# Performance work log

Hardware: AMD Instinct MI355X
Metric: run time of the kernel (lower is better)

The kernel has to match this reference:

```python
import jax, jax.numpy as jnp
import numpy as np

HEADS = 8
CH = 64  # channel_head
SCALE = CH ** -0.5


def rmsnorm2d(x, g):
    # F.normalize(x, dim=1) * g * sqrt(C)  (lucidrains conv RMSNorm)
    c = x.shape[1]
    n = jnp.sqrt(jnp.sum(x * x, axis=1, keepdims=True))
    return x / jnp.maximum(n, 1e-12) * g[None, :, None, None] * (c ** 0.5)


def setup_inputs() -> dict:
    key = jax.random.key(0)
    ks = jax.random.split(key, 3)
    B, C, H, W = 8, 512, 64, 64
    hidden = HEADS * CH  # 512
    x = jax.random.normal(ks[0], (B, C, H, W), dtype=jnp.float32)
    norm_g = jnp.ones((C,), dtype=jnp.float32)
    qkv_w = jax.random.normal(ks[1], (3 * hidden, C), dtype=jnp.float32) * 0.02
    ffn_w = jax.random.normal(ks[2], (C, hidden), dtype=jnp.float32) * 0.02
    ffn_b = jnp.zeros((C,), dtype=jnp.float32)
    ffn_norm_g = jnp.ones((C,), dtype=jnp.float32)
    return {"x": x, "norm_g": norm_g, "qkv_w": qkv_w, "ffn_w": ffn_w,
            "ffn_b": ffn_b, "ffn_norm_g": ffn_norm_g}


def reference(x, norm_g, qkv_w, ffn_w, ffn_b, ffn_norm_g):
    b, c, h, w = x.shape
    n = h * w
    residual = x
    xn = rmsnorm2d(x, norm_g)
    # 1x1 conv == channel matmul: [b, 3*hidden, h, w]
    qkv = jnp.einsum('bchw,oc->bohw', xn, qkv_w)
    q, k, v = jnp.split(qkv, 3, axis=1)

    def to_heads(t):
        # b (h c) x y -> b h (x y) c
        t = t.reshape(b, HEADS, CH, n)
        return jnp.transpose(t, (0, 1, 3, 2))  # [b, heads, n, ch]

    q, k, v = to_heads(q), to_heads(k), to_heads(v)
    q = jax.nn.softmax(q, axis=-1) * SCALE   # softmax over channel dim
    k = jax.nn.softmax(k, axis=-2)           # softmax over sequence dim
    attn = jnp.einsum('bhnc,bhnd->bhcd', k, v)    # [b, heads, ch, ch]
    out = jnp.einsum('bhnc,bhcd->bhnd', q, attn)  # [b, heads, n, ch]
    # b h (x y) c -> b (h c) x y
    out = jnp.transpose(out, (0, 1, 3, 2)).reshape(b, HEADS * CH, h, w)
    # ffn: 1x1 conv (with bias) + RMSNorm
    out = jnp.einsum('bchw,oc->bohw', out, ffn_w) + ffn_b[None, :, None, None]
    out = rmsnorm2d(out, ffn_norm_g)
    return out + residual
```

## Files before the change

kernel.cpp:

```cpp
#include <hip/hip_runtime.h>


typedef __bf16 bf16_t;
typedef __bf16 bf8 __attribute__((ext_vector_type(8)));
typedef float f32x4 __attribute__((ext_vector_type(4)));

#define NC 512
#define NP 4096
#define SQRTC 22.62741699796952f
#define QSCALE 0.125f
#define QSTRIDE  ((size_t)NC * NP)
#define KVSTRIDE ((size_t)1024 * NP)
#define LDC 136

__device__ inline unsigned short bfbits(__bf16 h) {
    return __builtin_bit_cast(unsigned short, h);
}

__device__ __forceinline__ void gload_lds16(const bf16_t* g, __bf16* l) {
    __builtin_amdgcn_global_load_lds(
        (const __attribute__((address_space(1))) void*)g,
        (__attribute__((address_space(3))) void*)l, 16, 0, 0);
}

__global__ __launch_bounds__(256) void
wconv_kernel(const float* __restrict__ qkv_w, const float* __restrict__ g,
             const float* __restrict__ ffn_w, bf16_t* __restrict__ Wg,
             bf16_t* __restrict__ Wf) {
    const int bx = blockIdx.x;
    if (bx < 768) {
        int i0 = (bx * 256 + threadIdx.x) * 4;
        float4 wv = *(const float4*)&qkv_w[i0];
        const float4 gv = *(const float4*)&g[i0 & 511];
        ushort4 o;
        o.x = bfbits((__bf16)(wv.x * gv.x));
        o.y = bfbits((__bf16)(wv.y * gv.y));
        o.z = bfbits((__bf16)(wv.z * gv.z));
        o.w = bfbits((__bf16)(wv.w * gv.w));
        *(ushort4*)&Wg[i0] = o;
    } else {
        int i0 = ((bx - 768) * 256 + threadIdx.x) * 4;
        float4 wv = *(const float4*)&ffn_w[i0];
        ushort4 o;
        o.x = bfbits((__bf16)wv.x);
        o.y = bfbits((__bf16)wv.y);
        o.z = bfbits((__bf16)wv.z);
        o.w = bfbits((__bf16)wv.w);
        *(ushort4*)&Wf[i0] = o;
    }
}

__global__ __launch_bounds__(512) void
norm_transpose_kernel(const float* __restrict__ x, bf16_t* __restrict__ xnT,
                      const float* __restrict__ qkv_w, const float* __restrict__ g,
                      const float* __restrict__ ffn_w, bf16_t* __restrict__ Wg,
                      bf16_t* __restrict__ Wf, int doW) {
    const int bl = blockIdx.y;
    const int p0 = blockIdx.x * 32;
    const int t = threadIdx.x;

    if (doW) {
        const int bid = blockIdx.y * 128 + blockIdx.x;
        if (bid < 512) {
            int i0 = bid * 2048 + t * 4;
            if (i0 < 786432) {
                float4 wv = *(const float4*)&qkv_w[i0];
                const float4 gv = *(const float4*)&g[i0 & 511];
                ushort4 o;
                o.x = bfbits((__bf16)(wv.x * gv.x));
                o.y = bfbits((__bf16)(wv.y * gv.y));
                o.z = bfbits((__bf16)(wv.z * gv.z));
                o.w = bfbits((__bf16)(wv.w * gv.w));
                *(ushort4*)&Wg[i0] = o;
            } else {
                int j0 = i0 - 786432;
                float4 wv = *(const float4*)&ffn_w[j0];
                ushort4 o;
                o.x = bfbits((__bf16)wv.x);
                o.y = bfbits((__bf16)wv.y);
                o.z = bfbits((__bf16)wv.z);
                o.w = bfbits((__bf16)wv.w);
                *(ushort4*)&Wf[j0] = o;
            }
        }
    }

    const float* xb = x + (size_t)bl * QSTRIDE;
    bf16_t* ob = xnT + (size_t)bl * QSTRIDE;

    const int cg = t & 7, r0 = t >> 3;
    f32x4 ss = {0.f, 0.f, 0.f, 0.f};
    #pragma unroll
    for (int k = 0; k < 8; ++k) {
        const int c = r0 + k * 64;
        float4 v = *(const float4*)&xb[(size_t)c * NP + p0 + cg * 4];
        ss.x += v.x * v.x; ss.y += v.y * v.y;
        ss.z += v.z * v.z; ss.w += v.w * v.w;
    }
    #pragma unroll
    for (int m = 8; m <= 32; m <<= 1) {
        ss.x += __shfl_xor(ss.x, m); ss.y += __shfl_xor(ss.y, m);
        ss.z += __shfl_xor(ss.z, m); ss.w += __shfl_xor(ss.w, m);
    }
    __shared__ float sP[8][34];
    __shared__ float sInv[32];
    const int w = t >> 6;
    if ((t & 63) < 8) {
        const int p = (t & 7) * 4;
        sP[w][p] = ss.x; sP[w][p + 1] = ss.y;
        sP[w][p + 2] = ss.z; sP[w][p + 3] = ss.w;
    }
    __syncthreads();
    if (t < 32) {
        float tot = 0.f;
        #pragma unroll
        for (int j = 0; j < 8; ++j) tot += sP[j][t];
        sInv[t] = SQRTC / fmaxf(sqrtf(tot), 1e-12f);
    }
    __syncthreads();

    __shared__ __bf16 sT[128][41];
    for (int cc = 0; cc < 512; cc += 128) {
        #pragma unroll
        for (int j = 0; j < 2; ++j) {
            int idx = t + j * 512;
            int cr = idx >> 3, pg = idx & 7;
            float4 v = *(const float4*)&xb[(size_t)(cc + cr) * NP + p0 + pg * 4];
            sT[cr][pg * 4 + 0] = (__bf16)(v.x * sInv[pg * 4 + 0]);
            sT[cr][pg * 4 + 1] = (__bf16)(v.y * sInv[pg * 4 + 1]);
            sT[cr][pg * 4 + 2] = (__bf16)(v.z * sInv[pg * 4 + 2]);
            sT[cr][pg * 4 + 3] = (__bf16)(v.w * sInv[pg * 4 + 3]);
        }
        __syncthreads();
        {
            int p = t >> 4, c8 = (t & 15) * 8;
            bf8 v;
            #pragma unroll
            for (int q = 0; q < 8; ++q) v[q] = sT[c8 + q][p];
            *(bf8*)&ob[(size_t)(p0 + p) * NC + cc + c8] = v;
        }
        __syncthreads();
    }
}

__global__ __launch_bounds__(256) void
gemm_qkv_kernel(const bf16_t* __restrict__ Wg, const bf16_t* __restrict__ xnT,
                bf16_t* __restrict__ qout, bf16_t* __restrict__ kvout) {
    const int bn = blockIdx.x, bm = blockIdx.y, b = blockIdx.z;
    const int t = threadIdx.x;
    const int w = t >> 6, ln = t & 63, quad = ln >> 4, l16 = ln & 15;
    const int wm = w >> 1, wn = w & 1;

    __shared__ __align__(16) __bf16 sAB[128 * LDC];
    __bf16* const sA = sAB;
    __bf16* const sB = sAB + 8192;

    f32x4 acc[4][4] = {};
    const bf16_t* Abase = Wg + (size_t)(bm * 128) * NC;
    const bf16_t* Bbase = xnT + (size_t)b * QSTRIDE + (size_t)(bn * 128) * NC;

    const int lrow = ln >> 3;
    const int lkc = ((ln & 7) ^ lrow) * 8;
    const int xr = l16 & 7;

    for (int kt = 0; kt < 8; ++kt) {
        const int k0 = kt * 64;
        #pragma unroll
        for (int i = 0; i < 4; ++i) {
            const int chunk = w * 4 + i;
            const int row = chunk * 8 + lrow;
            gload_lds16(Abase + (size_t)row * NC + k0 + lkc, &sA[chunk * 512]);
            gload_lds16(Bbase + (size_t)row * NC + k0 + lkc, &sB[chunk * 512]);
        }
        __syncthreads();
        #pragma unroll
        for (int ks = 0; ks < 2; ++ks) {
            bf8 af[4], bfr[4];
            const int kx = ((ks * 4 + quad) ^ xr) << 3;
            #pragma unroll
            for (int mi = 0; mi < 4; ++mi)
                af[mi] = *(const bf8*)&sA[(wm * 64 + mi * 16 + l16) * 64 + kx];
            #pragma unroll
            for (int ni = 0; ni < 4; ++ni)
                bfr[ni] = *(const bf8*)&sB[(wn * 64 + ni * 16 + l16) * 64 + kx];
            #pragma unroll
            for (int mi = 0; mi < 4; ++mi)
                #pragma unroll
                for (int ni = 0; ni < 4; ++ni)
                    acc[mi][ni] = __builtin_amdgcn_mfma_f32_16x16x32_bf16(
                        af[mi], bfr[ni], acc[mi][ni], 0, 0, 0);
        }
        __syncthreads();
    }

    const int p0 = bn * 128;
    if (bm < 4) {
        #pragma unroll
        for (int mi = 0; mi < 4; ++mi)
            #pragma unroll
            for (int ni = 0; ni < 4; ++ni)
                #pragma unroll
                for (int r = 0; r < 4; ++r)
                    sAB[(wn * 64 + ni * 16 + l16) * LDC +
                        wm * 64 + mi * 16 + quad * 4 + r] = (__bf16)acc[mi][ni][r];
        __syncthreads();
        {
            __bf16* rp = &sAB[(t & 127) * LDC + (t >> 7) * 64];
            float m = -1e30f;
            #pragma unroll
            for (int gg = 0; gg < 8; ++gg) {
                bf8 v = *(const bf8*)&rp[gg * 8];
                #pragma unroll
                for (int j = 0; j < 8; ++j) m = fmaxf(m, (float)v[j]);
            }
            float s = 0.f;
            #pragma unroll
            for (int gg = 0; gg < 8; ++gg) {
                bf8 v = *(const bf8*)&rp[gg * 8];
                #pragma unroll
                for (int j = 0; j < 8; ++j) s += __expf((float)v[j] - m);
            }
            const float inv = QSCALE / s;
            #pragma unroll
            for (int gg = 0; gg < 8; ++gg) {
                bf8 v = *(const bf8*)&rp[gg * 8];
                #pragma unroll
                for (int j = 0; j < 8; ++j)
                    v[j] = (__bf16)(__expf((float)v[j] - m) * inv);
                *(bf8*)&rp[gg * 8] = v;
            }
        }
        __syncthreads();
        bf16_t* qb = qout + (size_t)b * QSTRIDE;
        #pragma unroll
        for (int i = 0; i < 8; ++i) {
            int e = t + i * 256;
            int p = e >> 4, c8 = (e & 15) * 8;
            bf8 v = *(const bf8*)&sAB[p * LDC + c8];
            *(bf8*)&qb[(size_t)(p0 + p) * NC + bm * 128 + c8] = v;
        }
    } else {
        {
            const int rbase = wm * 64 + quad * 4;
            const int cbase = wn * 64 + l16;
            #pragma unroll
            for (int mi = 0; mi < 4; ++mi)
                #pragma unroll
                for (int ni = 0; ni < 4; ++ni)
                    #pragma unroll
                    for (int r = 0; r < 4; ++r)
                        sAB[(rbase + mi * 16 + r) * LDC + cbase + ni * 16] =
                            (__bf16)acc[mi][ni][r];
        }
        __syncthreads();
        bf16_t* kvb = kvout + (size_t)b * KVSTRIDE;
        #pragma unroll
        for (int i = 0; i < 8; ++i) {
            int e = t + i * 256;
            int rr = e >> 4, seg = (e & 15) * 8;
            bf8 v = *(const bf8*)&sAB[rr * LDC + seg];
            *(bf8*)&kvb[(size_t)(bm * 128 + rr - 512) * NP + p0 + seg] = v;
        }
    }
}

__global__ __launch_bounds__(256) void
kstats_kernel(const bf16_t* __restrict__ kv, float* __restrict__ kmax,
              float* __restrict__ kinv) {
    const int oc = blockIdx.x, b = blockIdx.y;
    const int t = threadIdx.x, w = t >> 6, ln = t & 63;

    const bf16_t* row = kv + (size_t)b * KVSTRIDE + (size_t)oc * NP;
    float v[16];
    bf8 x0 = *(const bf8*)&row[t * 8];
    bf8 x1 = *(const bf8*)&row[2048 + t * 8];
    #pragma unroll
    for (int j = 0; j < 8; ++j) { v[j] = (float)x0[j]; v[8 + j] = (float)x1[j]; }

    float m = v[0];
    #pragma unroll
    for (int j = 1; j < 16; ++j) m = fmaxf(m, v[j]);
    #pragma unroll
    for (int off = 32; off > 0; off >>= 1) m = fmaxf(m, __shfl_down(m, off));
    __shared__ float sR[4];
    __shared__ float sS[4];
    if (ln == 0) sR[w] = m;
    __syncthreads();
    m = fmaxf(fmaxf(sR[0], sR[1]), fmaxf(sR[2], sR[3]));

    float s = 0.f;
    #pragma unroll
    for (int j = 0; j < 16; ++j) s += __expf(v[j] - m);
    #pragma unroll
    for (int off = 32; off > 0; off >>= 1) s += __shfl_down(s, off);
    if (ln == 0) sS[w] = s;
    __syncthreads();
    if (t == 0) {
        kmax[b * 512 + oc] = m;
        kinv[b * 512 + oc] = 1.0f / (sS[0] + sS[1] + sS[2] + sS[3]);
    }
}

__global__ __launch_bounds__(256) void
attn_kernel(const bf16_t* __restrict__ kv, const float* __restrict__ kmax,
            float* __restrict__ attnP) {
    const int h = blockIdx.x, ks = blockIdx.y, b = blockIdx.z;
    const int t = threadIdx.x, w = t >> 6, ln = t & 63, quad = ln >> 4, l16 = ln & 15;

    const bf16_t* Kb = kv + (size_t)b * KVSTRIDE + (size_t)(h * 64) * NP;
    const bf16_t* Vb = kv + (size_t)b * KVSTRIDE + (size_t)(512 + h * 64 + w * 16) * NP;

    float km[4];
    #pragma unroll
    for (int mi = 0; mi < 4; ++mi) km[mi] = kmax[b * 512 + h * 64 + mi * 16 + l16];

    f32x4 acc[4] = {};
    const int pbase = ks * 512 + quad * 8;
    #pragma unroll 4
    for (int it = 0; it < 16; ++it) {
        const int p0 = pbase + it * 32;
        bf8 bfr = *(const bf8*)&Vb[(size_t)l16 * NP + p0];
        #pragma unroll
        for (int mi = 0; mi < 4; ++mi) {
            bf8 kr = *(const bf8*)&Kb[(size_t)(mi * 16 + l16) * NP + p0];
            bf8 af;
            #pragma unroll
            for (int j = 0; j < 8; ++j)
                af[j] = (__bf16)__expf((float)kr[j] - km[mi]);
            acc[mi] = __builtin_amdgcn_mfma_f32_16x16x32_bf16(af, bfr, acc[mi], 0, 0, 0);
        }
    }

    float* outp = attnP + (((size_t)(b * 8 + h) * 8 + ks) << 12);
    #pragma unroll
    for (int mi = 0; mi < 4; ++mi) {
        float4 v;
        v.x = acc[mi][0]; v.y = acc[mi][1]; v.z = acc[mi][2]; v.w = acc[mi][3];
        *(float4*)&outp[(w * 16 + l16) * 64 + mi * 16 + quad * 4] = v;
    }
}

__global__ __launch_bounds__(256) void
attnsum_kernel(const float* __restrict__ attnP, const float* __restrict__ kinv,
               bf16_t* __restrict__ attnF, float* __restrict__ ysq) {
    const int gtid = (blockIdx.x * 4 + blockIdx.y) * 256 + threadIdx.x;
    if (gtid < 8 * NP) ysq[gtid] = 0.f;

    const int bh = blockIdx.x;
    const int e0 = blockIdx.y * 1024 + threadIdx.x * 4;
    const float* ap = attnP + ((size_t)bh << 15);
    float4 s = {0.f, 0.f, 0.f, 0.f};
    #pragma unroll
    for (int ks = 0; ks < 8; ++ks) {
        float4 v = *(const float4*)&ap[(ks << 12) + e0];
        s.x += v.x; s.y += v.y; s.z += v.z; s.w += v.w;
    }
    const float* kvp = kinv + (bh >> 3) * 512 + (bh & 7) * 64;
    const int c = e0 & 63;
    ushort4 o;
    o.x = bfbits((__bf16)(s.x * kvp[c]));
    o.y = bfbits((__bf16)(s.y * kvp[c + 1]));
    o.z = bfbits((__bf16)(s.z * kvp[c + 2]));
    o.w = bfbits((__bf16)(s.w * kvp[c + 3]));
    *(ushort4*)&attnF[((size_t)bh << 12) + e0] = o;
}

__global__ __launch_bounds__(256) void
wmix_kernel(const bf16_t* __restrict__ Wf, const bf16_t* __restrict__ attnF,
            bf16_t* __restrict__ Wff) {
    const int om = blockIdx.x, h = blockIdx.y, b = blockIdx.z;
    const int t = threadIdx.x, w = t >> 6, ln = t & 63, quad = ln >> 4, l16 = ln & 15;

    __shared__ __bf16 sT[64][72];
    const bf16_t* aF = attnF + ((size_t)(b * 8 + h) << 12);
    #pragma unroll
    for (int i = 0; i < 2; ++i) {
        int e = t + i * 256;
        int d = e >> 3, c8 = (e & 7) * 8;
        bf8 v = *(const bf8*)&aF[d * 64 + c8];
        #pragma unroll
        for (int j = 0; j < 8; ++j) sT[c8 + j][d] = v[j];
    }
    __syncthreads();

    const int obase = om * 128 + w * 32;
    f32x4 acc[2][4] = {};
    #pragma unroll
    for (int kk = 0; kk < 2; ++kk) {
        bf8 af[2], bfr[4];
        #pragma unroll
        for (int mi = 0; mi < 2; ++mi)
            af[mi] = *(const bf8*)&Wf[(size_t)(obase + mi * 16 + l16) * NC +
                                      h * 64 + kk * 32 + quad * 8];
        #pragma unroll
        for (int ni = 0; ni < 4; ++ni)
            bfr[ni] = *(const bf8*)&sT[ni * 16 + l16][kk * 32 + quad * 8];
        #pragma unroll
        for (int mi = 0; mi < 2; ++mi)
            #pragma unroll
            for (int ni = 0; ni < 4; ++ni)
                acc[mi][ni] = __builtin_amdgcn_mfma_f32_16x16x32_bf16(
                    af[mi], bfr[ni], acc[mi][ni], 0, 0, 0);
    }
    bf16_t* outp = Wff + ((size_t)b << 18);
    #pragma unroll
    for (int mi = 0; mi < 2; ++mi)
        #pragma unroll
        for (int ni = 0; ni < 4; ++ni)
            #pragma unroll
            for (int r = 0; r < 4; ++r) {
                int o = obase + mi * 16 + quad * 4 + r;
                int c = ni * 16 + l16;
                outp[(size_t)o * NC + h * 64 + c] = (__bf16)acc[mi][ni][r];
            }
}

__global__ __launch_bounds__(256) void
gemm_ffn_kernel(const bf16_t* __restrict__ Wff, const bf16_t* __restrict__ qsm,
                const float* __restrict__ bias, float* __restrict__ out,
                float* __restrict__ ysq) {
    const int bn = blockIdx.x, bm = blockIdx.y, b = blockIdx.z;
    const int t = threadIdx.x;
    const int w = t >> 6, ln = t & 63, quad = ln >> 4, l16 = ln & 15;
    const int wm = w >> 1, wn = w & 1;

    __shared__ __align__(16) __bf16 sAB[128 * LDC];
    __bf16* const sA = sAB;
    __bf16* const sB = sAB + 8192;

    f32x4 acc[4][4] = {};
    const bf16_t* Abase = Wff + ((size_t)b << 18) + (size_t)(bm * 128) * NC;
    const bf16_t* Bbase = qsm + (size_t)b * QSTRIDE + (size_t)(bn * 128) * NC;

    const int lrow = ln >> 3;
    const int lkc = ((ln & 7) ^ lrow) * 8;
    const int xr = l16 & 7;

    for (int kt = 0; kt < 8; ++kt) {
        const int k0 = kt * 64;
        #pragma unroll
        for (int i = 0; i < 4; ++i) {
            const int chunk = w * 4 + i;
            const int row = chunk * 8 + lrow;
            gload_lds16(Abase + (size_t)row * NC + k0 + lkc, &sA[chunk * 512]);
            gload_lds16(Bbase + (size_t)row * NC + k0 + lkc, &sB[chunk * 512]);
        }
        __syncthreads();
        #pragma unroll
        for (int ks = 0; ks < 2; ++ks) {
            bf8 af[4], bfr[4];
            const int kx = ((ks * 4 + quad) ^ xr) << 3;
            #pragma unroll
            for (int mi = 0; mi < 4; ++mi)
                af[mi] = *(const bf8*)&sA[(wm * 64 + mi * 16 + l16) * 64 + kx];
            #pragma unroll
            for (int ni = 0; ni < 4; ++ni)
                bfr[ni] = *(const bf8*)&sB[(wn * 64 + ni * 16 + l16) * 64 + kx];
            #pragma unroll
            for (int mi = 0; mi < 4; ++mi)
                #pragma unroll
                for (int ni = 0; ni < 4; ++ni)
                    acc[mi][ni] = __builtin_amdgcn_mfma_f32_16x16x32_bf16(
                        af[mi], bfr[ni], acc[mi][ni], 0, 0, 0);
        }
        __syncthreads();
    }

    float* sq = ysq + (size_t)b * NP;
    const int p0 = bn * 128;
    const int rbase = wm * 64 + quad * 4;
    #pragma unroll
    for (int ni = 0; ni < 4; ++ni) {
        const int col = p0 + wn * 64 + ni * 16 + l16;
        float colsq = 0.f;
        #pragma unroll
        for (int mi = 0; mi < 4; ++mi)
            #pragma unroll
            for (int r = 0; r < 4; ++r) {
                float vf = acc[mi][ni][r] + bias[bm * 128 + rbase + mi * 16 + r];
                colsq += vf * vf;
            }
        colsq += __shfl_xor(colsq, 16);
        colsq += __shfl_xor(colsq, 32);
        if (quad == 0) atomicAdd(&sq[col], colsq);
    }

    float* sF = (float*)sAB;
    float* ob = out + (size_t)b * QSTRIDE;
    #pragma unroll
    for (int half = 0; half < 2; ++half) {
        __syncthreads();
        if (wm == half) {
            #pragma unroll
            for (int mi = 0; mi < 4; ++mi)
                #pragma unroll
                for (int ni = 0; ni < 4; ++ni)
                    #pragma unroll
                    for (int r = 0; r < 4; ++r)
                        sF[(quad * 4 + mi * 16 + r) * 136 + wn * 64 + ni * 16 + l16] =
                            acc[mi][ni][r] +
                            bias[bm * 128 + half * 64 + quad * 4 + mi * 16 + r];
        }
        __syncthreads();
        #pragma unroll
        for (int i = 0; i < 8; ++i) {
            int e = t + i * 256;
            int rr = e >> 5, c4 = (e & 31) * 4;
            float4 v = *(const float4*)&sF[rr * 136 + c4];
            *(float4*)&ob[(size_t)(bm * 128 + half * 64 + rr) * NP + p0 + c4] = v;
        }
    }
}

__global__ __launch_bounds__(256) void
final_kernel(float* __restrict__ out, const float* __restrict__ ysq,
             const float* __restrict__ g2, const float* __restrict__ x) {
    const int b = blockIdx.y;
    int idx = blockIdx.x * 256 + threadIdx.x;
    int o = idx >> 9;
    int p8 = (idx & 511) * 8;
    float* ob = out + (size_t)b * QSTRIDE;
    const float* xb = x + (size_t)b * QSTRIDE;
    const float* sq = ysq + (size_t)b * NP;

    float4 y0 = *(const float4*)&ob[(size_t)o * NP + p8];
    float4 y1 = *(const float4*)&ob[(size_t)o * NP + p8 + 4];
    float gv = g2[o] * SQRTC;
    float4 a = *(const float4*)&xb[(size_t)o * NP + p8];
    float4 b2 = *(const float4*)&xb[(size_t)o * NP + p8 + 4];
    float inb[8];
    #pragma unroll
    for (int j = 0; j < 8; ++j)
        inb[j] = 1.0f / fmaxf(sqrtf(sq[p8 + j]), 1e-12f);

    float4 r0, r1;
    r0.x = y0.x * inb[0] * gv + a.x;
    r0.y = y0.y * inb[1] * gv + a.y;
    r0.z = y0.z * inb[2] * gv + a.z;
    r0.w = y0.w * inb[3] * gv + a.w;
    r1.x = y1.x * inb[4] * gv + b2.x;
    r1.y = y1.y * inb[5] * gv + b2.y;
    r1.z = y1.z * inb[6] * gv + b2.z;
    r1.w = y1.w * inb[7] * gv + b2.w;
    *(float4*)&ob[(size_t)o * NP + p8] = r0;
    *(float4*)&ob[(size_t)o * NP + p8 + 4] = r1;
}

extern "C" void kernel_launch(void* const* d_in, const int* in_sizes, int n_in,
                              void* d_out, int out_size, void* d_ws, size_t ws_size,
                              hipStream_t stream) {
    const float* x     = (const float*)d_in[0];
    const float* g     = (const float*)d_in[1];
    const float* qkv_w = (const float*)d_in[2];
    const float* ffn_w = (const float*)d_in[3];
    const float* ffn_b = (const float*)d_in[4];
    const float* ffn_g = (const float*)d_in[5];
    float* out = (float*)d_out;
    bf16_t* kv = (bf16_t*)d_out;

    const size_t FULL_BYTES =
        (8 * QSTRIDE + 8 * QSTRIDE + 786432 + 262144) * sizeof(bf16_t) +
        (8 * 512 + 8 * 512 + 8 * (size_t)NP) * sizeof(float);
    const bool full = ws_size >= FULL_BYTES;

    bf16_t* q    = (bf16_t*)d_ws;
    bf16_t* xnT  = q + 8 * QSTRIDE;
    bf16_t* Wg   = xnT + (full ? 8 : 2) * QSTRIDE;
    float*  attnP = (float*)xnT;
    bf16_t* attnF = Wg;
    bf16_t* Wff  = xnT;
    bf16_t* Wf   = Wg + 786432;
    float*  kmax = (float*)(Wf + 262144);
    float*  kinv = kmax + 8 * 512;
    float*  ysq  = kinv + 8 * 512;

    if (full) {
        norm_transpose_kernel<<<dim3(128, 8), 512, 0, stream>>>(
            x, xnT, qkv_w, g, ffn_w, Wg, Wf, 1);
        gemm_qkv_kernel<<<dim3(32, 12, 8), 256, 0, stream>>>(Wg, xnT, q, kv);
    } else {
        wconv_kernel<<<dim3(1024), 256, 0, stream>>>(qkv_w, g, ffn_w, Wg, Wf);
        for (int c = 0; c < 4; ++c) {
            norm_transpose_kernel<<<dim3(128, 2), 512, 0, stream>>>(
                x + (size_t)(2 * c) * QSTRIDE, xnT,
                qkv_w, g, ffn_w, Wg, Wf, 0);
            gemm_qkv_kernel<<<dim3(32, 12, 2), 256, 0, stream>>>(
                Wg, xnT, q + (size_t)(2 * c) * QSTRIDE,
                kv + (size_t)(2 * c) * KVSTRIDE);
        }
    }

    kstats_kernel<<<dim3(512, 8), 256, 0, stream>>>(kv, kmax, kinv);
    attn_kernel<<<dim3(8, 8, 8), 256, 0, stream>>>(kv, kmax, attnP);
    attnsum_kernel<<<dim3(64, 4), 256, 0, stream>>>(attnP, kinv, attnF, ysq);
    wmix_kernel<<<dim3(4, 8, 8), 256, 0, stream>>>(Wf, attnF, Wff);
    gemm_ffn_kernel<<<dim3(32, 4, 8), 256, 0, stream>>>(Wff, q, ffn_b, out, ysq);
    final_kernel<<<dim3(1024, 8), 256, 0, stream>>>(out, ysq, ffn_g, x);
}
```

Measured before the change: 304.3 us.

## Fold attnsum into wmix, zero ysq in attn, store FFN output as bf16

On the full-workspace path, the separate attnsum launch is removed. The partial-attention reduction and kinv scaling move into wmix_kernel, and attn_kernel now zeroes ysq. The FFN GEMM writes its pre-norm output as bf16 to workspace instead of fp32 to the output buffer, and the column sum-of-squares is computed from the rounded values. This halves the intermediate write and read in final_kernel at the cost of bf16 rounding of the pre-norm activations, and it places Wff in the kv region.

```diff
diff --git a/kernel.cpp b/kernel.cpp
--- a/kernel.cpp
+++ b/kernel.cpp
@@ -303,9 +303,12 @@
 
 __global__ __launch_bounds__(256) void
 attn_kernel(const bf16_t* __restrict__ kv, const float* __restrict__ kmax,
-            float* __restrict__ attnP) {
+            float* __restrict__ attnP, float* __restrict__ ysq) {
     const int h = blockIdx.x, ks = blockIdx.y, b = blockIdx.z;
     const int t = threadIdx.x, w = t >> 6, ln = t & 63, quad = ln >> 4, l16 = ln & 15;
+
+    const int zid = ((b * 8 + ks) * 8 + h) * 256 + t;
+    if (zid < 8 * NP) ysq[zid] = 0.f;
 
     const bf16_t* Kb = kv + (size_t)b * KVSTRIDE + (size_t)(h * 64) * NP;
     const bf16_t* Vb = kv + (size_t)b * KVSTRIDE + (size_t)(512 + h * 64 + w * 16) * NP;
@@ -366,20 +369,43 @@
 }
 
 __global__ __launch_bounds__(256) void
-wmix_kernel(const bf16_t* __restrict__ Wf, const bf16_t* __restrict__ attnF,
-            bf16_t* __restrict__ Wff) {
+wmix_kernel(const bf16_t* __restrict__ Wf, const float* __restrict__ attnP,
+            const float* __restrict__ kinv, const bf16_t* __restrict__ attnF,
+            bf16_t* __restrict__ Wff, int selfsum) {
     const int om = blockIdx.x, h = blockIdx.y, b = blockIdx.z;
     const int t = threadIdx.x, w = t >> 6, ln = t & 63, quad = ln >> 4, l16 = ln & 15;
 
     __shared__ __bf16 sT[64][72];
-    const bf16_t* aF = attnF + ((size_t)(b * 8 + h) << 12);
-    #pragma unroll
-    for (int i = 0; i < 2; ++i) {
-        int e = t + i * 256;
-        int d = e >> 3, c8 = (e & 7) * 8;
-        bf8 v = *(const bf8*)&aF[d * 64 + c8];
-        #pragma unroll
-        for (int j = 0; j < 8; ++j) sT[c8 + j][d] = v[j];
+    if (selfsum) {
+        const float* ap = attnP + ((size_t)(b * 8 + h) << 15);
+        const float* kvp = kinv + b * 512 + h * 64;
+        #pragma unroll
+        for (int i = 0; i < 2; ++i) {
+            int e = t + i * 256;
+            int d = e >> 3, c8 = (e & 7) * 8;
+            float s[8] = {};
+            #pragma unroll
+            for (int ks = 0; ks < 8; ++ks) {
+                const float* pp = &ap[(ks << 12) + d * 64 + c8];
+                float4 v0 = *(const float4*)pp;
+                float4 v1 = *(const float4*)(pp + 4);
+                s[0] += v0.x; s[1] += v0.y; s[2] += v0.z; s[3] += v0.w;
+                s[4] += v1.x; s[5] += v1.y; s[6] += v1.z; s[7] += v1.w;
+            }
+            #pragma unroll
+            for (int j = 0; j < 8; ++j)
+                sT[c8 + j][d] = (__bf16)(s[j] * kvp[c8 + j]);
+        }
+    } else {
+        const bf16_t* aF = attnF + ((size_t)(b * 8 + h) << 12);
+        #pragma unroll
+        for (int i = 0; i < 2; ++i) {
+            int e = t + i * 256;
+            int d = e >> 3, c8 = (e & 7) * 8;
+            bf8 v = *(const bf8*)&aF[d * 64 + c8];
+            #pragma unroll
+            for (int j = 0; j < 8; ++j) sT[c8 + j][d] = v[j];
+        }
     }
     __syncthreads();
 
@@ -417,8 +443,8 @@
 
 __global__ __launch_bounds__(256) void
 gemm_ffn_kernel(const bf16_t* __restrict__ Wff, const bf16_t* __restrict__ qsm,
-                const float* __restrict__ bias, float* __restrict__ out,
-                float* __restrict__ ysq) {
+                const float* __restrict__ bias, float* __restrict__ outf,
+                bf16_t* __restrict__ ybf16, float* __restrict__ ysq, int ybf) {
     const int bn = blockIdx.x, bm = blockIdx.y, b = blockIdx.z;
     const int t = threadIdx.x;
     const int w = t >> 6, ln = t & 63, quad = ln >> 4, l16 = ln & 15;
@@ -469,52 +495,84 @@
     float* sq = ysq + (size_t)b * NP;
     const int p0 = bn * 128;
     const int rbase = wm * 64 + quad * 4;
-    #pragma unroll
-    for (int ni = 0; ni < 4; ++ni) {
-        const int col = p0 + wn * 64 + ni * 16 + l16;
-        float colsq = 0.f;
-        #pragma unroll
-        for (int mi = 0; mi < 4; ++mi)
-            #pragma unroll
-            for (int r = 0; r < 4; ++r) {
-                float vf = acc[mi][ni][r] + bias[bm * 128 + rbase + mi * 16 + r];
-                colsq += vf * vf;
-            }
-        colsq += __shfl_xor(colsq, 16);
-        colsq += __shfl_xor(colsq, 32);
-        if (quad == 0) atomicAdd(&sq[col], colsq);
-    }
-
-    float* sF = (float*)sAB;
-    float* ob = out + (size_t)b * QSTRIDE;
-    #pragma unroll
-    for (int half = 0; half < 2; ++half) {
-        __syncthreads();
-        if (wm == half) {
-            #pragma unroll
-            for (int mi = 0; mi < 4; ++mi)
-                #pragma unroll
-                for (int ni = 0; ni < 4; ++ni)
-                    #pragma unroll
-                    for (int r = 0; r < 4; ++r)
-                        sF[(quad * 4 + mi * 16 + r) * 136 + wn * 64 + ni * 16 + l16] =
-                            acc[mi][ni][r] +
-                            bias[bm * 128 + half * 64 + quad * 4 + mi * 16 + r];
-        }
-        __syncthreads();
+
+    if (ybf) {
+        #pragma unroll
+        for (int ni = 0; ni < 4; ++ni) {
+            const int col = p0 + wn * 64 + ni * 16 + l16;
+            float colsq = 0.f;
+            #pragma unroll
+            for (int mi = 0; mi < 4; ++mi) {
+                #pragma unroll
+                for (int r = 0; r < 4; ++r) {
+                    const int row = bm * 128 + rbase + mi * 16 + r;
+                    __bf16 vb = (__bf16)(acc[mi][ni][r] + bias[row]);
+                    sAB[(rbase + mi * 16 + r) * LDC + wn * 64 + ni * 16 + l16] = vb;
+                    float vf = (float)vb;
+                    colsq += vf * vf;
+                }
+            }
+            colsq += __shfl_xor(colsq, 16);
+            colsq += __shfl_xor(colsq, 32);
+            if (quad == 0) atomicAdd(&sq[col], colsq);
+        }
+        __syncthreads();
+        bf16_t* yb = ybf16 + (size_t)b * QSTRIDE;
         #pragma unroll
         for (int i = 0; i < 8; ++i) {
             int e = t + i * 256;
-            int rr = e >> 5, c4 = (e & 31) * 4;
-            float4 v = *(const float4*)&sF[rr * 136 + c4];
-            *(float4*)&ob[(size_t)(bm * 128 + half * 64 + rr) * NP + p0 + c4] = v;
-        }
-    }
-}
-
-__global__ __launch_bounds__(256) void
-final_kernel(float* __restrict__ out, const float* __restrict__ ysq,
-             const float* __restrict__ g2, const float* __restrict__ x) {
+            int rr = e >> 4, seg = (e & 15) * 8;
+            bf8 v = *(const bf8*)&sAB[rr * LDC + seg];
+            *(bf8*)&yb[(size_t)(bm * 128 + rr) * NP + p0 + seg] = v;
+        }
+    } else {
+        #pragma unroll
+        for (int ni = 0; ni < 4; ++ni) {
+            const int col = p0 + wn * 64 + ni * 16 + l16;
+            float colsq = 0.f;
+            #pragma unroll
+            for (int mi = 0; mi < 4; ++mi)
+                #pragma unroll
+                for (int r = 0; r < 4; ++r) {
+                    float vf = acc[mi][ni][r] + bias[bm * 128 + rbase + mi * 16 + r];
+                    colsq += vf * vf;
+                }
+            colsq += __shfl_xor(colsq, 16);
+            colsq += __shfl_xor(colsq, 32);
+            if (quad == 0) atomicAdd(&sq[col], colsq);
+        }
+        float* sF = (float*)sAB;
+        float* ob = outf + (size_t)b * QSTRIDE;
+        #pragma unroll
+        for (int half = 0; half < 2; ++half) {
+            __syncthreads();
+            if (wm == half) {
+                #pragma unroll
+                for (int mi = 0; mi < 4; ++mi)
+                    #pragma unroll
+                    for (int ni = 0; ni < 4; ++ni)
+                        #pragma unroll
+                        for (int r = 0; r < 4; ++r)
+                            sF[(quad * 4 + mi * 16 + r) * 136 + wn * 64 + ni * 16 + l16] =
+                                acc[mi][ni][r] +
+                                bias[bm * 128 + half * 64 + quad * 4 + mi * 16 + r];
+            }
+            __syncthreads();
+            #pragma unroll
+            for (int i = 0; i < 8; ++i) {
+                int e = t + i * 256;
+                int rr = e >> 5, c4 = (e & 31) * 4;
+                float4 v = *(const float4*)&sF[rr * 136 + c4];
+                *(float4*)&ob[(size_t)(bm * 128 + half * 64 + rr) * NP + p0 + c4] = v;
+            }
+        }
+    }
+}
+
+__global__ __launch_bounds__(256) void
+final_kernel(float* __restrict__ out, const bf16_t* __restrict__ ybf16,
+             const float* __restrict__ ysq, const float* __restrict__ g2,
+             const float* __restrict__ x, int ybf) {
     const int b = blockIdx.y;
     int idx = blockIdx.x * 256 + threadIdx.x;
     int o = idx >> 9;
@@ -523,8 +581,6 @@
     const float* xb = x + (size_t)b * QSTRIDE;
     const float* sq = ysq + (size_t)b * NP;
 
-    float4 y0 = *(const float4*)&ob[(size_t)o * NP + p8];
-    float4 y1 = *(const float4*)&ob[(size_t)o * NP + p8 + 4];
     float gv = g2[o] * SQRTC;
     float4 a = *(const float4*)&xb[(size_t)o * NP + p8];
     float4 b2 = *(const float4*)&xb[(size_t)o * NP + p8 + 4];
@@ -533,15 +589,28 @@
     for (int j = 0; j < 8; ++j)
         inb[j] = 1.0f / fmaxf(sqrtf(sq[p8 + j]), 1e-12f);
 
+    float y[8];
+    if (ybf) {
+        const bf16_t* yb = ybf16 + (size_t)b * QSTRIDE;
+        bf8 yv = *(const bf8*)&yb[(size_t)o * NP + p8];
+        #pragma unroll
+        for (int j = 0; j < 8; ++j) y[j] = (float)yv[j];
+    } else {
+        float4 y0 = *(const float4*)&ob[(size_t)o * NP + p8];
+        float4 y1 = *(const float4*)&ob[(size_t)o * NP + p8 + 4];
+        y[0] = y0.x; y[1] = y0.y; y[2] = y0.z; y[3] = y0.w;
+        y[4] = y1.x; y[5] = y1.y; y[6] = y1.z; y[7] = y1.w;
+    }
+
     float4 r0, r1;
-    r0.x = y0.x * inb[0] * gv + a.x;
-    r0.y = y0.y * inb[1] * gv + a.y;
-    r0.z = y0.z * inb[2] * gv + a.z;
-    r0.w = y0.w * inb[3] * gv + a.w;
-    r1.x = y1.x * inb[4] * gv + b2.x;
-    r1.y = y1.y * inb[5] * gv + b2.y;
-    r1.z = y1.z * inb[6] * gv + b2.z;
-    r1.w = y1.w * inb[7] * gv + b2.w;
+    r0.x = y[0] * inb[0] * gv + a.x;
+    r0.y = y[1] * inb[1] * gv + a.y;
+    r0.z = y[2] * inb[2] * gv + a.z;
+    r0.w = y[3] * inb[3] * gv + a.w;
+    r1.x = y[4] * inb[4] * gv + b2.x;
+    r1.y = y[5] * inb[5] * gv + b2.y;
+    r1.z = y[6] * inb[6] * gv + b2.z;
+    r1.w = y[7] * inb[7] * gv + b2.w;
     *(float4*)&ob[(size_t)o * NP + p8] = r0;
     *(float4*)&ob[(size_t)o * NP + p8 + 4] = r1;
 }
@@ -567,8 +636,10 @@
     bf16_t* xnT  = q + 8 * QSTRIDE;
     bf16_t* Wg   = xnT + (full ? 8 : 2) * QSTRIDE;
     float*  attnP = (float*)xnT;
+    bf16_t* y16  = xnT;
     bf16_t* attnF = Wg;
-    bf16_t* Wff  = xnT;
+    bf16_t* WffC = xnT;
+    bf16_t* WffF = kv;
     bf16_t* Wf   = Wg + 786432;
     float*  kmax = (float*)(Wf + 262144);
     float*  kinv = kmax + 8 * 512;
@@ -578,6 +649,14 @@
         norm_transpose_kernel<<<dim3(128, 8), 512, 0, stream>>>(
             x, xnT, qkv_w, g, ffn_w, Wg, Wf, 1);
         gemm_qkv_kernel<<<dim3(32, 12, 8), 256, 0, stream>>>(Wg, xnT, q, kv);
+        kstats_kernel<<<dim3(512, 8), 256, 0, stream>>>(kv, kmax, kinv);
+        attn_kernel<<<dim3(8, 8, 8), 256, 0, stream>>>(kv, kmax, attnP, ysq);
+        wmix_kernel<<<dim3(4, 8, 8), 256, 0, stream>>>(
+            Wf, attnP, kinv, nullptr, WffF, 1);
+        gemm_ffn_kernel<<<dim3(32, 4, 8), 256, 0, stream>>>(
+            WffF, q, ffn_b, nullptr, y16, ysq, 1);
+        final_kernel<<<dim3(1024, 8), 256, 0, stream>>>(
+            out, y16, ysq, ffn_g, x, 1);
     } else {
         wconv_kernel<<<dim3(1024), 256, 0, stream>>>(qkv_w, g, ffn_w, Wg, Wf);
         for (int c = 0; c < 4; ++c) {
@@ -588,12 +667,14 @@
                 Wg, xnT, q + (size_t)(2 * c) * QSTRIDE,
                 kv + (size_t)(2 * c) * KVSTRIDE);
         }
-    }
-
-    kstats_kernel<<<dim3(512, 8), 256, 0, stream>>>(kv, kmax, kinv);
-    attn_kernel<<<dim3(8, 8, 8), 256, 0, stream>>>(kv, kmax, attnP);
-    attnsum_kernel<<<dim3(64, 4), 256, 0, stream>>>(attnP, kinv, attnF, ysq);
-    wmix_kernel<<<dim3(4, 8, 8), 256, 0, stream>>>(Wf, attnF, Wff);
-    gemm_ffn_kernel<<<dim3(32, 4, 8), 256, 0, stream>>>(Wff, q, ffn_b, out, ysq);
-    final_kernel<<<dim3(1024, 8), 256, 0, stream>>>(out, ysq, ffn_g, x);
-}
+        kstats_kernel<<<dim3(512, 8), 256, 0, stream>>>(kv, kmax, kinv);
+        attn_kernel<<<dim3(8, 8, 8), 256, 0, stream>>>(kv, kmax, attnP, ysq);
+        attnsum_kernel<<<dim3(64, 4), 256, 0, stream>>>(attnP, kinv, attnF, ysq);
+        wmix_kernel<<<dim3(4, 8, 8), 256, 0, stream>>>(
+            Wf, attnP, kinv, attnF, WffC, 0);
+        gemm_ffn_kernel<<<dim3(32, 4, 8), 256, 0, stream>>>(
+            WffC, q, ffn_b, out, nullptr, ysq, 0);
+        final_kernel<<<dim3(1024, 8), 256, 0, stream>>>(
+            out, nullptr, ysq, ffn_g, x, 0);
+    }
+}
```

Measured after the change: 294.3 us. -3.3%, faster.
